# Optimization experiments

Hardware: AMD Instinct MI355X
Metric: run time of the kernel (lower is better)

The kernel has to match this reference:

```python
import jax, jax.numpy as jnp
import numpy as np
from jax import lax

B, L, S, D = 2, 8, 512, 256


def setup_inputs() -> dict:
    key = jax.random.key(0)
    ks = jax.random.split(key, 12)
    s = 1.0 / np.sqrt(D)
    return {
        "features": jax.random.normal(ks[0], (B, L, S, D), jnp.float32),
        "source_features": jax.random.normal(ks[1], (B, S, D), jnp.float32),
        "target_features": jax.random.normal(ks[2], (B, S, D), jnp.float32),
        # GRU params (torch layout: [3D, D] with gate order r, z, n)
        "W_ih": jax.random.uniform(ks[3], (3 * D, D), jnp.float32, -s, s),
        "W_hh": jax.random.uniform(ks[4], (3 * D, D), jnp.float32, -s, s),
        "b_ih": jax.random.uniform(ks[5], (3 * D,), jnp.float32, -s, s),
        "b_hh": jax.random.uniform(ks[6], (3 * D,), jnp.float32, -s, s),
        # causal_predictor: Linear(2D, D) -> ReLU -> Linear(D, D) -> Sigmoid
        "W1": jax.random.uniform(ks[7], (D, 2 * D), jnp.float32, -s, s),
        "b1": jax.random.uniform(ks[8], (D,), jnp.float32, -s, s),
        "W2": jax.random.uniform(ks[9], (D, D), jnp.float32, -s, s),
        "b2": jax.random.uniform(ks[10], (D,), jnp.float32, -s, s),
    }


def _gru(x, W_ih, W_hh, b_ih, b_hh):
    # x: [N, T, D] batch-first; returns all hidden states [N, T, D]
    N, T, d = x.shape
    gx = jnp.einsum('ntd,gd->ntg', x, W_ih) + b_ih  # [N, T, 3D]

    def step(h, gx_t):
        gh = h @ W_hh.T + b_hh
        r = jax.nn.sigmoid(gx_t[:, :d] + gh[:, :d])
        z = jax.nn.sigmoid(gx_t[:, d:2 * d] + gh[:, d:2 * d])
        n = jnp.tanh(gx_t[:, 2 * d:] + r * gh[:, 2 * d:])
        h_new = (1.0 - z) * n + z * h
        return h_new, h_new

    h0 = jnp.zeros((N, d), x.dtype)
    _, outs = lax.scan(step, h0, jnp.swapaxes(gx, 0, 1))  # [T, N, D]
    return jnp.swapaxes(outs, 0, 1)


def reference(features, source_features, target_features,
              W_ih, W_hh, b_ih, b_hh, W1, b1, W2, b2):
    b, l, s, d = features.shape
    fdim = jnp.float32(d)

    # --- track_feature_evolution, vectorized over seq positions ---
    # per-position GRU over the layer axis == one GRU over a B*S batch
    x = jnp.transpose(features, (0, 2, 1, 3)).reshape(b * s, l, d)
    evolution_out = _gru(x, W_ih, W_hh, b_ih, b_hh).reshape(b, s, l, d)

    prev = features[:, :-1]            # [B, L-1, S, D]
    nxt = features[:, 1:]
    eps = jnp.float32(1e-8)
    na = jnp.maximum(jnp.linalg.norm(prev, axis=-1), eps)
    nb = jnp.maximum(jnp.linalg.norm(nxt, axis=-1), eps)
    stability = (jnp.sum(prev * nxt, axis=-1) / (na * nb)).mean(axis=0)  # [L-1, S]

    act = jnp.sum((features > 0.1).astype(jnp.float32), axis=-1)  # [B, L, S]
    emergence = (act[:, 1:] - act[:, :-1]).mean(axis=0) / fdim    # [L-1, S]
    decay = (act[:, :-1] - act[:, 1:]).mean(axis=0) / fdim        # [L-1, S]

    # --- compute_causal_strength ---
    # combined[b,s,i,:D] = source[b,s,:]; combined[b,s,i,D+k] = target[b,s,i] (all k)
    # first Linear(2D->D) therefore splits into:  source @ W1a^T  +  target_i * sum_k W1b[:,k]
    W1a = W1[:, :d]                     # [D, D]
    wb = jnp.sum(W1[:, d:], axis=1)     # [D]
    A = jnp.einsum('bsd,od->bso', source_features, W1a) + b1  # [B, S, D]
    h = A[:, :, None, :] + target_features[:, :, :, None] * wb  # [B, S, D(i), D(o)]
    h = jax.nn.relu(h)
    out2 = jax.nn.sigmoid(jnp.einsum('bsio,po->bsip', h, W2) + b2)  # [B, S, D, D]
    causal_matrix = out2.mean(axis=(0, 1))  # [D, D]

    return stability, emergence, decay, causal_matrix, evolution_out
```

## Files before the change

kernel.cpp:

```cpp
#include <hip/hip_runtime.h>
#include <hip/hip_bf16.h>
#include <stdint.h>

typedef unsigned short u16;
typedef __bf16 v8bf __attribute__((ext_vector_type(8)));
typedef float f32x4 __attribute__((ext_vector_type(4)));

#define WS_WB    0u
#define WS_WIHB  4096u
#define WS_WHHB  397312u
#define WS_W2B   790528u
#define WS_A     921600u
#define WS_GX    2097152u
#define WS_PART  27262976u

#define OUT_STAB   0
#define OUT_EMER   3584
#define OUT_DECAY  7168
#define OUT_CAUSAL 10752
#define OUT_EVO    76288

__device__ __forceinline__ u16 f2bfu(float f){
    union { float f; uint32_t u; } v; v.f = f;
    uint32_t u = v.u;
    return (u16)((u + 0x7fffu + ((u >> 16) & 1u)) >> 16);
}
__device__ __forceinline__ float sigmoidf_fast(float x){
    float e = __builtin_amdgcn_exp2f(-1.4426950408889634f * x);
    return __builtin_amdgcn_rcpf(1.0f + e);
}
__device__ __forceinline__ float tanhf_fast(float x){
    float e = __builtin_amdgcn_exp2f(-2.8853900817779268f * x);
    return __builtin_amdgcn_rcpf(1.0f + e) * 2.0f - 1.0f;
}
__device__ __forceinline__ f32x4 mfma16(v8bf a, v8bf b, f32x4 c){
    return __builtin_amdgcn_mfma_f32_16x16x32_bf16(a, b, c, 0, 0, 0);
}
__device__ __forceinline__ v8bf cvt8(const float* p){
    float4 a = *(const float4*)p;
    float4 b = *(const float4*)(p + 4);
    v8bf r;
    r[0] = (__bf16)a.x; r[1] = (__bf16)a.y; r[2] = (__bf16)a.z; r[3] = (__bf16)a.w;
    r[4] = (__bf16)b.x; r[5] = (__bf16)b.y; r[6] = (__bf16)b.z; r[7] = (__bf16)b.w;
    return r;
}

__global__ __launch_bounds__(256) void k_pre(
        const float* __restrict__ feat, const float* __restrict__ src,
        const float* __restrict__ Wih,  const float* __restrict__ Whh,
        const float* __restrict__ W1,   const float* __restrict__ b1,
        const float* __restrict__ W2,
        u16* __restrict__ wihb, u16* __restrict__ whhb, u16* __restrict__ w2b,
        float* __restrict__ wb, float* __restrict__ A, float* __restrict__ out){
    const int bid = blockIdx.x, tid = threadIdx.x;
    if (bid < 64){
        const int bs0 = bid * 16;
        const int lane = tid & 63, w = tid >> 6;
        const int l15 = lane & 15, quad = lane >> 4;
        v8bf xa[8];
        for (int k = 0; k < 8; k++)
            xa[k] = cvt8(&src[(bs0 + l15) * 256 + k * 32 + quad * 8]);
        f32x4 acc[4];
        for (int nt = 0; nt < 4; nt++) acc[nt] = (f32x4){0.f, 0.f, 0.f, 0.f};
        for (int k = 0; k < 8; k++){
            int d0 = k * 32 + quad * 8;
            for (int nt = 0; nt < 4; nt++){
                int o = w * 64 + nt * 16 + l15;
                v8bf bfr = cvt8(&W1[o * 512 + d0]);
                acc[nt] = mfma16(xa[k], bfr, acc[nt]);
            }
        }
        for (int nt = 0; nt < 4; nt++){
            int o = w * 64 + nt * 16 + l15;
            float bb = b1[o];
            for (int r = 0; r < 4; r++)
                A[(bs0 + quad * 4 + r) * 256 + o] = acc[nt][r] + bb;
        }
    } else if (bid < 960){
        const int pair = (bid - 64) * 4 + (tid >> 6);
        const int l = pair >> 9, s = pair & 511;
        const int lane = tid & 63;
        float stab = 0.f, emer = 0.f;
        for (int b = 0; b < 2; b++){
            const float* p = feat + ((size_t)((b * 8 + l) * 512 + s)) * 256;
            const float* n = feat + ((size_t)((b * 8 + l + 1) * 512 + s)) * 256;
            float4 pv = *(const float4*)(p + lane * 4);
            float4 nv = *(const float4*)(n + lane * 4);
            float dot = pv.x * nv.x + pv.y * nv.y + pv.z * nv.z + pv.w * nv.w;
            float na2 = pv.x * pv.x + pv.y * pv.y + pv.z * pv.z + pv.w * pv.w;
            float nb2 = nv.x * nv.x + nv.y * nv.y + nv.z * nv.z + nv.w * nv.w;
            float ap = ((pv.x > 0.1f) ? 1.f : 0.f) + ((pv.y > 0.1f) ? 1.f : 0.f)
                     + ((pv.z > 0.1f) ? 1.f : 0.f) + ((pv.w > 0.1f) ? 1.f : 0.f);
            float an = ((nv.x > 0.1f) ? 1.f : 0.f) + ((nv.y > 0.1f) ? 1.f : 0.f)
                     + ((nv.z > 0.1f) ? 1.f : 0.f) + ((nv.w > 0.1f) ? 1.f : 0.f);
            for (int off = 32; off > 0; off >>= 1){
                dot += __shfl_xor(dot, off);
                na2 += __shfl_xor(na2, off);
                nb2 += __shfl_xor(nb2, off);
                ap  += __shfl_xor(ap,  off);
                an  += __shfl_xor(an,  off);
            }
            float na = fmaxf(__builtin_sqrtf(na2), 1e-8f);
            float nb = fmaxf(__builtin_sqrtf(nb2), 1e-8f);
            stab += dot / (na * nb);
            emer += (an - ap);
        }
        if (lane == 0){
            int o = l * 512 + s;
            float e = emer * 0.5f * (1.0f / 256.0f);
            out[OUT_STAB  + o] = stab * 0.5f;
            out[OUT_EMER  + o] = e;
            out[OUT_DECAY + o] = -e;
        }
    } else {
        int idx8 = (bid - 960) * 256 + tid;
        if (idx8 < 57344){
            const float* srcp;
            u16* dstp;
            if (idx8 < 24576){ srcp = Wih + idx8 * 8;             dstp = wihb + idx8 * 8; }
            else if (idx8 < 49152){ int i = idx8 - 24576; srcp = Whh + i * 8; dstp = whhb + i * 8; }
            else { int i = idx8 - 49152; srcp = W2 + i * 8; dstp = w2b + i * 8; }
            float4 a = *(const float4*)srcp;
            float4 b = *(const float4*)(srcp + 4);
            union { u16 h[8]; uint4 v; } pk;
            pk.h[0] = f2bfu(a.x); pk.h[1] = f2bfu(a.y);
            pk.h[2] = f2bfu(a.z); pk.h[3] = f2bfu(a.w);
            pk.h[4] = f2bfu(b.x); pk.h[5] = f2bfu(b.y);
            pk.h[6] = f2bfu(b.z); pk.h[7] = f2bfu(b.w);
            *(uint4*)dstp = pk.v;
        } else if (idx8 < 57600){
            int o = idx8 - 57344;
            float s = 0.f;
            const float4* p = (const float4*)&W1[o * 512 + 256];
            for (int j = 0; j < 64; j++){
                float4 v = p[j];
                s += v.x + v.y + v.z + v.w;
            }
            wb[o] = s;
        }
    }
}

__global__ __launch_bounds__(256, 2) void k_mid(
        const float* __restrict__ feat, const u16* __restrict__ wihb,
        const float* __restrict__ bih,  float* __restrict__ gxws,
        const float* __restrict__ Aws,  const float* __restrict__ wbws,
        const u16* __restrict__ w2b,    const float* __restrict__ tgt,
        const float* __restrict__ b2,   float* __restrict__ part){
    __shared__ __align__(16) unsigned char smem[69632];
    const int tid = threadIdx.x, lane = tid & 63, w = tid >> 6;
    const int l15 = lane & 15, quad = lane >> 4;

    if (blockIdx.x < 384){
        const int mb = blockIdx.x / 6, nb = blockIdx.x % 6;
        u16* blds = (u16*)smem;

        {
            int r = tid >> 1, half = tid & 1;
            const uint4* gsrc = (const uint4*)&wihb[(nb * 128 + r) * 256 + half * 128];
            for (int j = 0; j < 16; j++){
                int c = half * 16 + j;
                *(uint4*)&blds[r * 256 + ((c ^ (r & 31)) << 3)] = gsrc[j];
            }
        }

        v8bf af[2][8];
        for (int mt = 0; mt < 2; mt++){
            int r = mb * 128 + w * 32 + mt * 16 + l15;
            int n = r >> 3, t = r & 7;
            int b = n >> 9, s = n & 511;
            const float* xp = feat + ((size_t)((b * 8 + t) * 512 + s)) * 256;
            for (int kk = 0; kk < 8; kk++)
                af[mt][kk] = cvt8(xp + kk * 32 + quad * 8);
        }
        __syncthreads();

        f32x4 acc[2][8];
        for (int mt = 0; mt < 2; mt++) for (int nt = 0; nt < 8; nt++)
            acc[mt][nt] = (f32x4){0.f, 0.f, 0.f, 0.f};
        for (int kk = 0; kk < 8; kk++){
            int kq = kk * 4 + quad;
            for (int nt = 0; nt < 8; nt++){
                int pl = nt * 16 + l15;
                v8bf bf = *(const v8bf*)&blds[pl * 256 + ((kq ^ (pl & 31)) << 3)];
                acc[0][nt] = mfma16(af[0][kk], bf, acc[0][nt]);
                acc[1][nt] = mfma16(af[1][kk], bf, acc[1][nt]);
            }
        }
        for (int nt = 0; nt < 8; nt++){
            int g = nb * 128 + nt * 16 + l15;
            float bias = bih[g];
            for (int mt = 0; mt < 2; mt++)
                for (int rr = 0; rr < 4; rr++){
                    int row = mb * 128 + w * 32 + mt * 16 + quad * 4 + rr;
                    gxws[(size_t)row * 768 + g] = acc[mt][nt][rr] + bias;
                }
        }
        return;
    }

    const int bidc = blockIdx.x - 384;
    const int chunk = bidc >> 2, q = bidc & 3;
    const int i0 = (q & 1) * 128, p0 = (q >> 1) * 128;

    u16*  w2s  = (u16*)smem;
    float* a_db = (float*)(smem + 65536);
    float* t_db = (float*)(smem + 67584);
    float* wb_s = (float*)(smem + 68608);

    {
        int r = tid >> 1, half = tid & 1;
        const uint4* gsrc = (const uint4*)&w2b[(p0 + r) * 256 + half * 128];
        for (int j = 0; j < 16; j++){
            int c = half * 16 + j;
            *(uint4*)&w2s[r * 256 + ((c ^ (r & 31)) << 3)] = gsrc[j];
        }
    }
    wb_s[tid] = wbws[tid];
    a_db[tid] = Aws[chunk * 8 * 256 + tid];
    if (tid < 128) t_db[tid] = tgt[(chunk * 8) * 256 + i0 + tid];

    float bb[8];
    for (int nt = 0; nt < 8; nt++) bb[nt] = b2[p0 + nt * 16 + l15];

    f32x4 sig[2][8];
    for (int mt = 0; mt < 2; mt++) for (int nt = 0; nt < 8; nt++)
        sig[mt][nt] = (f32x4){0.f, 0.f, 0.f, 0.f};

    for (int ss = 0; ss < 8; ss++){
        __syncthreads();
        if (ss < 7){
            int nb = (ss + 1) & 1;
            a_db[nb * 256 + tid] = Aws[(chunk * 8 + ss + 1) * 256 + tid];
            if (tid < 128) t_db[nb * 128 + tid] = tgt[(chunk * 8 + ss + 1) * 256 + i0 + tid];
        }
        const int cb = ss & 1;
        float tv0 = t_db[cb * 128 + w * 32 + l15];
        float tv1 = t_db[cb * 128 + w * 32 + 16 + l15];

        f32x4 acc[2][8];
        for (int mt = 0; mt < 2; mt++) for (int nt = 0; nt < 8; nt++)
            acc[mt][nt] = (f32x4){0.f, 0.f, 0.f, 0.f};

        for (int k = 0; k < 8; k++){
            const int o0 = k * 32 + quad * 8;
            const int kq = k * 4 + quad;
            float4 a0  = *(const float4*)&a_db[cb * 256 + o0];
            float4 a1  = *(const float4*)&a_db[cb * 256 + o0 + 4];
            float4 w0  = *(const float4*)&wb_s[o0];
            float4 w1v = *(const float4*)&wb_s[o0 + 4];
            v8bf afr0, afr1;
            {
                float t = tv0;
                afr0[0] = (__bf16)fmaxf(fmaf(t, w0.x,  a0.x), 0.f);
                afr0[1] = (__bf16)fmaxf(fmaf(t, w0.y,  a0.y), 0.f);
                afr0[2] = (__bf16)fmaxf(fmaf(t, w0.z,  a0.z), 0.f);
                afr0[3] = (__bf16)fmaxf(fmaf(t, w0.w,  a0.w), 0.f);
                afr0[4] = (__bf16)fmaxf(fmaf(t, w1v.x, a1.x), 0.f);
                afr0[5] = (__bf16)fmaxf(fmaf(t, w1v.y, a1.y), 0.f);
                afr0[6] = (__bf16)fmaxf(fmaf(t, w1v.z, a1.z), 0.f);
                afr0[7] = (__bf16)fmaxf(fmaf(t, w1v.w, a1.w), 0.f);
            }
            {
                float t = tv1;
                afr1[0] = (__bf16)fmaxf(fmaf(t, w0.x,  a0.x), 0.f);
                afr1[1] = (__bf16)fmaxf(fmaf(t, w0.y,  a0.y), 0.f);
                afr1[2] = (__bf16)fmaxf(fmaf(t, w0.z,  a0.z), 0.f);
                afr1[3] = (__bf16)fmaxf(fmaf(t, w0.w,  a0.w), 0.f);
                afr1[4] = (__bf16)fmaxf(fmaf(t, w1v.x, a1.x), 0.f);
                afr1[5] = (__bf16)fmaxf(fmaf(t, w1v.y, a1.y), 0.f);
                afr1[6] = (__bf16)fmaxf(fmaf(t, w1v.z, a1.z), 0.f);
                afr1[7] = (__bf16)fmaxf(fmaf(t, w1v.w, a1.w), 0.f);
            }
            for (int nt = 0; nt < 8; nt++){
                int pl = nt * 16 + l15;
                v8bf bfr = *(const v8bf*)&w2s[pl * 256 + ((kq ^ (pl & 31)) << 3)];
                acc[0][nt] = mfma16(afr0, bfr, acc[0][nt]);
                acc[1][nt] = mfma16(afr1, bfr, acc[1][nt]);
            }
        }
        for (int mt = 0; mt < 2; mt++)
            for (int nt = 0; nt < 8; nt++)
                for (int r = 0; r < 4; r++)
                    sig[mt][nt][r] += sigmoidf_fast(acc[mt][nt][r] + bb[nt]);
    }

    float* pp = part + (size_t)chunk * 65536;
    for (int mt = 0; mt < 2; mt++)
        for (int r = 0; r < 4; r++){
            int i = i0 + w * 32 + mt * 16 + quad * 4 + r;
            for (int nt = 0; nt < 8; nt++){
                int p = p0 + nt * 16 + l15;
                pp[i * 256 + p] = sig[mt][nt][r];
            }
        }
}

__global__ __launch_bounds__(512) void k_final(
        const float* __restrict__ gxws, const u16* __restrict__ whhb,
        const float* __restrict__ bhh, const float* __restrict__ part,
        float* __restrict__ out){
    if (blockIdx.x >= 64){
        const int idx = (blockIdx.x - 64) * 512 + threadIdx.x;
        float s = 0.f;
        for (int c = 0; c < 128; c++)
            s += part[(size_t)c * 65536 + idx];
        out[OUT_CAUSAL + idx] = s * (1.0f / 1024.0f);
        return;
    }
    const int n0 = blockIdx.x * 16;
    const int tid = threadIdx.x, lane = tid & 63, wv = tid >> 6;
    const int l15 = lane & 15, quad = lane >> 4;
    const int g0 = wv * 96;

    __shared__ float h_lds[16 * 260];
    __shared__ float g_lds[16 * 776];

    v8bf wreg[3][8];
    for (int nt = 0; nt < 3; nt++)
        for (int k = 0; k < 8; k++)
            wreg[nt][k] = *(const v8bf*)&whhb[(g0 + nt * 16 + l15) * 256 + k * 32 + quad * 8];

    float bias[6];
    for (int nt = 0; nt < 6; nt++) bias[nt] = bhh[g0 + nt * 16 + l15];

    for (int e = tid; e < 16 * 260; e += 512) h_lds[e] = 0.f;

    const int seq = tid >> 5, d0 = (tid & 31) * 8;
    const float* gxbase = gxws + (size_t)(n0 + seq) * 8 * 768 + d0;
    float* evobase = out + OUT_EVO + (size_t)(n0 + seq) * 8 * 256 + d0;
    __syncthreads();

    for (int t = 0; t < 8; t++){
        v8bf ha[8];
        for (int k = 0; k < 8; k++)
            ha[k] = cvt8(&h_lds[l15 * 260 + k * 32 + quad * 8]);
        f32x4 acc[6];
        for (int nt = 0; nt < 6; nt++) acc[nt] = (f32x4){0.f, 0.f, 0.f, 0.f};
        for (int k = 0; k < 8; k++){
            int dk = k * 32 + quad * 8;
            acc[0] = mfma16(ha[k], wreg[0][k], acc[0]);
            acc[1] = mfma16(ha[k], wreg[1][k], acc[1]);
            acc[2] = mfma16(ha[k], wreg[2][k], acc[2]);
            for (int nt = 3; nt < 6; nt++){
                v8bf bf = *(const v8bf*)&whhb[(g0 + nt * 16 + l15) * 256 + dk];
                acc[nt] = mfma16(ha[k], bf, acc[nt]);
            }
        }
        for (int nt = 0; nt < 6; nt++){
            int g = g0 + nt * 16 + l15;
            for (int rr = 0; rr < 4; rr++)
                g_lds[(quad * 4 + rr) * 776 + g] = acc[nt][rr] + bias[nt];
        }
        const float* gxp = gxbase + (size_t)t * 768;
        float4 x0a = *(const float4*)(gxp);
        float4 x0b = *(const float4*)(gxp + 4);
        float4 x1a = *(const float4*)(gxp + 256);
        float4 x1b = *(const float4*)(gxp + 260);
        float4 x2a = *(const float4*)(gxp + 512);
        float4 x2b = *(const float4*)(gxp + 516);
        __syncthreads();
        {
            const float* gh = &g_lds[seq * 776];
            float* hp = &h_lds[seq * 260 + d0];
            float4 g0a = *(const float4*)&gh[d0];
            float4 g0b = *(const float4*)&gh[d0 + 4];
            float4 g1a = *(const float4*)&gh[256 + d0];
            float4 g1b = *(const float4*)&gh[260 + d0];
            float4 g2a = *(const float4*)&gh[512 + d0];
            float4 g2b = *(const float4*)&gh[516 + d0];
            float4 h0 = *(const float4*)hp;
            float4 h1 = *(const float4*)(hp + 4);
            float gxr[8] = {x0a.x, x0a.y, x0a.z, x0a.w, x0b.x, x0b.y, x0b.z, x0b.w};
            float gxz[8] = {x1a.x, x1a.y, x1a.z, x1a.w, x1b.x, x1b.y, x1b.z, x1b.w};
            float gxn[8] = {x2a.x, x2a.y, x2a.z, x2a.w, x2b.x, x2b.y, x2b.z, x2b.w};
            float ghr[8] = {g0a.x, g0a.y, g0a.z, g0a.w, g0b.x, g0b.y, g0b.z, g0b.w};
            float ghz[8] = {g1a.x, g1a.y, g1a.z, g1a.w, g1b.x, g1b.y, g1b.z, g1b.w};
            float ghn[8] = {g2a.x, g2a.y, g2a.z, g2a.w, g2b.x, g2b.y, g2b.z, g2b.w};
            float hold[8] = {h0.x, h0.y, h0.z, h0.w, h1.x, h1.y, h1.z, h1.w};
            float hn[8];
            #pragma unroll
            for (int j = 0; j < 8; j++){
                float r  = sigmoidf_fast(gxr[j] + ghr[j]);
                float z  = sigmoidf_fast(gxz[j] + ghz[j]);
                float nn = tanhf_fast(fmaf(r, ghn[j], gxn[j]));
                hn[j] = (1.f - z) * nn + z * hold[j];
            }
            float4 v0 = {hn[0], hn[1], hn[2], hn[3]};
            float4 v1 = {hn[4], hn[5], hn[6], hn[7]};
            *(float4*)hp       = v0;
            *(float4*)(hp + 4) = v1;
            float* ep = evobase + (size_t)t * 256;
            *(float4*)ep       = v0;
            *(float4*)(ep + 4) = v1;
        }
        __syncthreads();
    }
}

extern "C" void kernel_launch(void* const* d_in, const int* in_sizes, int n_in,
                              void* d_out, int out_size, void* d_ws, size_t ws_size,
                              hipStream_t stream){
    const float* feat = (const float*)d_in[0];
    const float* src  = (const float*)d_in[1];
    const float* tgt  = (const float*)d_in[2];
    const float* Wih  = (const float*)d_in[3];
    const float* Whh  = (const float*)d_in[4];
    const float* bih  = (const float*)d_in[5];
    const float* bhh  = (const float*)d_in[6];
    const float* W1   = (const float*)d_in[7];
    const float* b1   = (const float*)d_in[8];
    const float* W2   = (const float*)d_in[9];
    const float* b2   = (const float*)d_in[10];
    float* out = (float*)d_out;
    char* ws = (char*)d_ws;

    float* wb   = (float*)(ws + WS_WB);
    u16*   wihb = (u16*)(ws + WS_WIHB);
    u16*   whhb = (u16*)(ws + WS_WHHB);
    u16*   w2b  = (u16*)(ws + WS_W2B);
    float* Aws  = (float*)(ws + WS_A);
    float* gxws = (float*)(ws + WS_GX);
    float* part = (float*)(ws + WS_PART);

    k_pre  <<<1185, 256, 0, stream>>>(feat, src, Wih, Whh, W1, b1, W2,
                                      wihb, whhb, w2b, wb, Aws, out);
    k_mid  <<<896,  256, 0, stream>>>(feat, wihb, bih, gxws,
                                      Aws, wb, w2b, tgt, b2, part);
    k_final<<<192,  512, 0, stream>>>(gxws, whhb, bhh, part, out);
}
```

Baseline: 219.9 us.

## Rebalance kernels: move stats to mid kernel, store gx in bf16, halve GRU tile

Moves the stability/emergence/decay reduction from the pre kernel into the mid kernel, so it runs alongside the causal and gx GEMM blocks, and reorders the block dispatch so causal blocks come first. Stores the precomputed GRU input gates as bf16 to halve workspace traffic. Halves the sequences per k_final block (8 instead of 16) to double its grid, though half the threads sit idle in the elementwise step. This risks extra rounding error in gx and wasted MFMA rows in the 16-row tiles.

```diff
diff --git a/kernel.cpp b/kernel.cpp
--- a/kernel.cpp
+++ b/kernel.cpp
@@ -25,6 +25,12 @@
     uint32_t u = v.u;
     return (u16)((u + 0x7fffu + ((u >> 16) & 1u)) >> 16);
 }
+__device__ __forceinline__ float hi2f(uint32_t w){
+    union { uint32_t u; float f; } v; v.u = w & 0xFFFF0000u; return v.f;
+}
+__device__ __forceinline__ float lo2f(uint32_t w){
+    union { uint32_t u; float f; } v; v.u = w << 16; return v.f;
+}
 __device__ __forceinline__ float sigmoidf_fast(float x){
     float e = __builtin_amdgcn_exp2f(-1.4426950408889634f * x);
     return __builtin_amdgcn_rcpf(1.0f + e);
@@ -46,12 +52,12 @@
 }
 
 __global__ __launch_bounds__(256) void k_pre(
-        const float* __restrict__ feat, const float* __restrict__ src,
+        const float* __restrict__ src,
         const float* __restrict__ Wih,  const float* __restrict__ Whh,
         const float* __restrict__ W1,   const float* __restrict__ b1,
         const float* __restrict__ W2,
         u16* __restrict__ wihb, u16* __restrict__ whhb, u16* __restrict__ w2b,
-        float* __restrict__ wb, float* __restrict__ A, float* __restrict__ out){
+        float* __restrict__ wb, float* __restrict__ A){
     const int bid = blockIdx.x, tid = threadIdx.x;
     if (bid < 64){
         const int bs0 = bid * 16;
@@ -76,44 +82,8 @@
             for (int r = 0; r < 4; r++)
                 A[(bs0 + quad * 4 + r) * 256 + o] = acc[nt][r] + bb;
         }
-    } else if (bid < 960){
-        const int pair = (bid - 64) * 4 + (tid >> 6);
-        const int l = pair >> 9, s = pair & 511;
-        const int lane = tid & 63;
-        float stab = 0.f, emer = 0.f;
-        for (int b = 0; b < 2; b++){
-            const float* p = feat + ((size_t)((b * 8 + l) * 512 + s)) * 256;
-            const float* n = feat + ((size_t)((b * 8 + l + 1) * 512 + s)) * 256;
-            float4 pv = *(const float4*)(p + lane * 4);
-            float4 nv = *(const float4*)(n + lane * 4);
-            float dot = pv.x * nv.x + pv.y * nv.y + pv.z * nv.z + pv.w * nv.w;
-            float na2 = pv.x * pv.x + pv.y * pv.y + pv.z * pv.z + pv.w * pv.w;
-            float nb2 = nv.x * nv.x + nv.y * nv.y + nv.z * nv.z + nv.w * nv.w;
-            float ap = ((pv.x > 0.1f) ? 1.f : 0.f) + ((pv.y > 0.1f) ? 1.f : 0.f)
-                     + ((pv.z > 0.1f) ? 1.f : 0.f) + ((pv.w > 0.1f) ? 1.f : 0.f);
-            float an = ((nv.x > 0.1f) ? 1.f : 0.f) + ((nv.y > 0.1f) ? 1.f : 0.f)
-                     + ((nv.z > 0.1f) ? 1.f : 0.f) + ((nv.w > 0.1f) ? 1.f : 0.f);
-            for (int off = 32; off > 0; off >>= 1){
-                dot += __shfl_xor(dot, off);
-                na2 += __shfl_xor(na2, off);
-                nb2 += __shfl_xor(nb2, off);
-                ap  += __shfl_xor(ap,  off);
-                an  += __shfl_xor(an,  off);
-            }
-            float na = fmaxf(__builtin_sqrtf(na2), 1e-8f);
-            float nb = fmaxf(__builtin_sqrtf(nb2), 1e-8f);
-            stab += dot / (na * nb);
-            emer += (an - ap);
-        }
-        if (lane == 0){
-            int o = l * 512 + s;
-            float e = emer * 0.5f * (1.0f / 256.0f);
-            out[OUT_STAB  + o] = stab * 0.5f;
-            out[OUT_EMER  + o] = e;
-            out[OUT_DECAY + o] = -e;
-        }
     } else {
-        int idx8 = (bid - 960) * 256 + tid;
+        int idx8 = (bid - 64) * 256 + tid;
         if (idx8 < 57344){
             const float* srcp;
             u16* dstp;
@@ -143,16 +113,56 @@
 
 __global__ __launch_bounds__(256, 2) void k_mid(
         const float* __restrict__ feat, const u16* __restrict__ wihb,
-        const float* __restrict__ bih,  float* __restrict__ gxws,
+        const float* __restrict__ bih,  u16* __restrict__ gxb,
         const float* __restrict__ Aws,  const float* __restrict__ wbws,
         const u16* __restrict__ w2b,    const float* __restrict__ tgt,
-        const float* __restrict__ b2,   float* __restrict__ part){
+        const float* __restrict__ b2,   float* __restrict__ part,
+        float* __restrict__ out){
     __shared__ __align__(16) unsigned char smem[69632];
     const int tid = threadIdx.x, lane = tid & 63, w = tid >> 6;
     const int l15 = lane & 15, quad = lane >> 4;
 
-    if (blockIdx.x < 384){
-        const int mb = blockIdx.x / 6, nb = blockIdx.x % 6;
+    if (blockIdx.x >= 896){
+        const int pair = (blockIdx.x - 896) * 4 + (tid >> 6);
+        const int l = pair >> 9, s = pair & 511;
+        float stab = 0.f, emer = 0.f;
+        for (int b = 0; b < 2; b++){
+            const float* p = feat + ((size_t)((b * 8 + l) * 512 + s)) * 256;
+            const float* n = feat + ((size_t)((b * 8 + l + 1) * 512 + s)) * 256;
+            float4 pv = *(const float4*)(p + lane * 4);
+            float4 nv = *(const float4*)(n + lane * 4);
+            float dot = pv.x * nv.x + pv.y * nv.y + pv.z * nv.z + pv.w * nv.w;
+            float na2 = pv.x * pv.x + pv.y * pv.y + pv.z * pv.z + pv.w * pv.w;
+            float nb2 = nv.x * nv.x + nv.y * nv.y + nv.z * nv.z + nv.w * nv.w;
+            float ap = ((pv.x > 0.1f) ? 1.f : 0.f) + ((pv.y > 0.1f) ? 1.f : 0.f)
+                     + ((pv.z > 0.1f) ? 1.f : 0.f) + ((pv.w > 0.1f) ? 1.f : 0.f);
+            float an = ((nv.x > 0.1f) ? 1.f : 0.f) + ((nv.y > 0.1f) ? 1.f : 0.f)
+                     + ((nv.z > 0.1f) ? 1.f : 0.f) + ((nv.w > 0.1f) ? 1.f : 0.f);
+            for (int off = 32; off > 0; off >>= 1){
+                dot += __shfl_xor(dot, off);
+                na2 += __shfl_xor(na2, off);
+                nb2 += __shfl_xor(nb2, off);
+                ap  += __shfl_xor(ap,  off);
+                an  += __shfl_xor(an,  off);
+            }
+            float na = fmaxf(__builtin_sqrtf(na2), 1e-8f);
+            float nb = fmaxf(__builtin_sqrtf(nb2), 1e-8f);
+            stab += dot / (na * nb);
+            emer += (an - ap);
+        }
+        if ((lane & 63) == 0){
+            int o = l * 512 + s;
+            float e = emer * 0.5f * (1.0f / 256.0f);
+            out[OUT_STAB  + o] = stab * 0.5f;
+            out[OUT_EMER  + o] = e;
+            out[OUT_DECAY + o] = -e;
+        }
+        return;
+    }
+
+    if (blockIdx.x >= 512){
+        const int gid = blockIdx.x - 512;
+        const int mb = gid / 6, nb = gid % 6;
         u16* blds = (u16*)smem;
 
         {
@@ -193,13 +203,13 @@
             for (int mt = 0; mt < 2; mt++)
                 for (int rr = 0; rr < 4; rr++){
                     int row = mb * 128 + w * 32 + mt * 16 + quad * 4 + rr;
-                    gxws[(size_t)row * 768 + g] = acc[mt][nt][rr] + bias;
+                    gxb[(size_t)row * 768 + g] = f2bfu(acc[mt][nt][rr] + bias);
                 }
         }
         return;
     }
 
-    const int bidc = blockIdx.x - 384;
+    const int bidc = blockIdx.x;
     const int chunk = bidc >> 2, q = bidc & 3;
     const int i0 = (q & 1) * 128, p0 = (q >> 1) * 128;
 
@@ -297,18 +307,18 @@
 }
 
 __global__ __launch_bounds__(512) void k_final(
-        const float* __restrict__ gxws, const u16* __restrict__ whhb,
+        const u16* __restrict__ gxb, const u16* __restrict__ whhb,
         const float* __restrict__ bhh, const float* __restrict__ part,
         float* __restrict__ out){
-    if (blockIdx.x >= 64){
-        const int idx = (blockIdx.x - 64) * 512 + threadIdx.x;
+    if (blockIdx.x >= 128){
+        const int idx = (blockIdx.x - 128) * 512 + threadIdx.x;
         float s = 0.f;
         for (int c = 0; c < 128; c++)
             s += part[(size_t)c * 65536 + idx];
         out[OUT_CAUSAL + idx] = s * (1.0f / 1024.0f);
         return;
     }
-    const int n0 = blockIdx.x * 16;
+    const int n0 = blockIdx.x * 8;
     const int tid = threadIdx.x, lane = tid & 63, wv = tid >> 6;
     const int l15 = lane & 15, quad = lane >> 4;
     const int g0 = wv * 96;
@@ -327,8 +337,6 @@
     for (int e = tid; e < 16 * 260; e += 512) h_lds[e] = 0.f;
 
     const int seq = tid >> 5, d0 = (tid & 31) * 8;
-    const float* gxbase = gxws + (size_t)(n0 + seq) * 8 * 768 + d0;
-    float* evobase = out + OUT_EVO + (size_t)(n0 + seq) * 8 * 256 + d0;
     __syncthreads();
 
     for (int t = 0; t < 8; t++){
@@ -352,15 +360,15 @@
             for (int rr = 0; rr < 4; rr++)
                 g_lds[(quad * 4 + rr) * 776 + g] = acc[nt][rr] + bias[nt];
         }
-        const float* gxp = gxbase + (size_t)t * 768;
-        float4 x0a = *(const float4*)(gxp);
-        float4 x0b = *(const float4*)(gxp + 4);
-        float4 x1a = *(const float4*)(gxp + 256);
-        float4 x1b = *(const float4*)(gxp + 260);
-        float4 x2a = *(const float4*)(gxp + 512);
-        float4 x2b = *(const float4*)(gxp + 516);
+        uint4 xr, xz, xn;
+        if (tid < 256){
+            const u16* gxp = gxb + ((size_t)(n0 + seq) * 8 + t) * 768 + d0;
+            xr = *(const uint4*)(gxp);
+            xz = *(const uint4*)(gxp + 256);
+            xn = *(const uint4*)(gxp + 512);
+        }
         __syncthreads();
-        {
+        if (tid < 256){
             const float* gh = &g_lds[seq * 776];
             float* hp = &h_lds[seq * 260 + d0];
             float4 g0a = *(const float4*)&gh[d0];
@@ -371,9 +379,12 @@
             float4 g2b = *(const float4*)&gh[516 + d0];
             float4 h0 = *(const float4*)hp;
             float4 h1 = *(const float4*)(hp + 4);
-            float gxr[8] = {x0a.x, x0a.y, x0a.z, x0a.w, x0b.x, x0b.y, x0b.z, x0b.w};
-            float gxz[8] = {x1a.x, x1a.y, x1a.z, x1a.w, x1b.x, x1b.y, x1b.z, x1b.w};
-            float gxn[8] = {x2a.x, x2a.y, x2a.z, x2a.w, x2b.x, x2b.y, x2b.z, x2b.w};
+            float gxr[8] = {lo2f(xr.x), hi2f(xr.x), lo2f(xr.y), hi2f(xr.y),
+                            lo2f(xr.z), hi2f(xr.z), lo2f(xr.w), hi2f(xr.w)};
+            float gxz[8] = {lo2f(xz.x), hi2f(xz.x), lo2f(xz.y), hi2f(xz.y),
+                            lo2f(xz.z), hi2f(xz.z), lo2f(xz.w), hi2f(xz.w)};
+            float gxn[8] = {lo2f(xn.x), hi2f(xn.x), lo2f(xn.y), hi2f(xn.y),
+                            lo2f(xn.z), hi2f(xn.z), lo2f(xn.w), hi2f(xn.w)};
             float ghr[8] = {g0a.x, g0a.y, g0a.z, g0a.w, g0b.x, g0b.y, g0b.z, g0b.w};
             float ghz[8] = {g1a.x, g1a.y, g1a.z, g1a.w, g1b.x, g1b.y, g1b.z, g1b.w};
             float ghn[8] = {g2a.x, g2a.y, g2a.z, g2a.w, g2b.x, g2b.y, g2b.z, g2b.w};
@@ -390,7 +401,7 @@
             float4 v1 = {hn[4], hn[5], hn[6], hn[7]};
             *(float4*)hp       = v0;
             *(float4*)(hp + 4) = v1;
-            float* ep = evobase + (size_t)t * 256;
+            float* ep = out + OUT_EVO + ((size_t)(n0 + seq) * 8 + t) * 256 + d0;
             *(float4*)ep       = v0;
             *(float4*)(ep + 4) = v1;
         }
@@ -420,12 +431,12 @@
     u16*   whhb = (u16*)(ws + WS_WHHB);
     u16*   w2b  = (u16*)(ws + WS_W2B);
     float* Aws  = (float*)(ws + WS_A);
-    float* gxws = (float*)(ws + WS_GX);
+    u16*   gxb  = (u16*)(ws + WS_GX);
     float* part = (float*)(ws + WS_PART);
 
-    k_pre  <<<1185, 256, 0, stream>>>(feat, src, Wih, Whh, W1, b1, W2,
-                                      wihb, whhb, w2b, wb, Aws, out);
-    k_mid  <<<896,  256, 0, stream>>>(feat, wihb, bih, gxws,
-                                      Aws, wb, w2b, tgt, b2, part);
-    k_final<<<192,  512, 0, stream>>>(gxws, whhb, bhh, part, out);
-}
+    k_pre  <<<289,  256, 0, stream>>>(src, Wih, Whh, W1, b1, W2,
+                                      wihb, whhb, w2b, wb, Aws);
+    k_mid  <<<1792, 256, 0, stream>>>(feat, wihb, bih, gxb,
+                                      Aws, wb, w2b, tgt, b2, part, out);
+    k_final<<<256,  512, 0, stream>>>(gxb, whhb, bhh, part, out);
+}
```

Result: faster. 214.2 us (-2.6%).
